# Kernel optimization log

Measured on AMD Instinct MI355X. Metric: run time of the kernel, lower is better.

Reference implementation:

```python
import jax, jax.numpy as jnp
import numpy as np
import math

CS = 8       # cell_size
NBINS = 8
SIGMA = 1.0
IMG = 224
BATCH = 256
TWO_PI = 2.0 * math.pi


def setup_inputs() -> dict:
    key = jax.random.key(0)
    x = jax.random.normal(key, (BATCH, 3, IMG, IMG), dtype=jnp.float32)
    coords = jnp.arange(CS, dtype=jnp.float32) - (CS - 1) / 2.0
    xx, yy = jnp.meshgrid(coords, coords, indexing='ij')
    gauss = jnp.exp(-(xx ** 2 + yy ** 2) / (2.0 * SIGMA ** 2)).reshape(1, CS * CS)
    kx = jnp.array([[-1., 0., 1.], [-2., 0., 2.], [-1., 0., 1.]], dtype=jnp.float32).reshape(1, 1, 3, 3)
    ky = jnp.array([[-1., -2., -1.], [0., 0., 0.], [1., 2., 1.]], dtype=jnp.float32).reshape(1, 1, 3, 3)
    return {"x": x, "gauss": gauss, "kx": kx, "ky": ky}


def _conv(im, k):
    # NCHW conv, padding=1, stride=1 (matches F.conv2d(..., padding=1))
    return jax.lax.conv_general_dilated(
        im, k, window_strides=(1, 1), padding=[(1, 1), (1, 1)],
        dimension_numbers=('NCHW', 'OIHW', 'NCHW'))


def reference(x, gauss, kx, ky):
    bs, _, H, W = x.shape
    gray = 0.2989 * x[:, 0:1] + 0.587 * x[:, 1:2] + 0.114 * x[:, 2:3]  # [bs,1,H,W]
    gx = _conv(gray, kx)
    gy = _conv(gray, ky)
    mag = jnp.sqrt(gx ** 2 + gy ** 2 + 1e-6)
    ang = jnp.mod(jnp.arctan2(gy, gx), TWO_PI)
    Hc, Wc = H // CS, W // CS
    n_cells = Hc * Wc

    def to_cells(a):
        # [bs,1,H,W] -> [bs*n_cells, CS*CS], within-cell order (kh,kw) row-major
        # matching F.unfold's kernel-position ordering.
        return a.reshape(bs, Hc, CS, Wc, CS).transpose(0, 1, 3, 2, 4).reshape(bs * n_cells, CS * CS)

    mags = to_cells(mag) * gauss  # gauss broadcasts over kernel positions
    angs = to_cells(ang)

    bin_w = TWO_PI / NBINS
    idx = (angs / bin_w).astype(jnp.int32) % NBINS  # [bs*n_cells, CS*CS]

    N = bs * n_cells
    hist = jnp.zeros((N, NBINS), dtype=mags.dtype)
    hist = hist.at[jnp.arange(N)[:, None], idx].add(mags)  # scatter_add per cell
    hist = hist.reshape(bs, n_cells * NBINS)
    hist = hist / (jnp.linalg.norm(hist, axis=1, keepdims=True) + 1e-6)
    return hist
```

## Files before the change

### kernel.cpp

```cpp
#include <hip/hip_runtime.h>
#include <math.h>

#define NBINS 8
#define IMG 224
#define HC 28
#define OUTPER (HC*HC*NBINS)
#define BATCH 256
#define PL (IMG*IMG)

__global__ __launch_bounds__(256) void hog_main_kernel(
    const float* __restrict__ x, const float* __restrict__ gauss,
    float* __restrict__ out, float* __restrict__ partial)
{
    const int tid  = threadIdx.x;
    const int wv   = tid >> 6;
    const int lane = tid & 63;
    const int bc   = blockIdx.x;
    const int b    = bc / HC;
    const int cr   = bc - b * HC;
    const int r0   = cr * 8;
    const int c0   = wv * 64;
    const int c    = c0 + lane;
    const int cl   = c > IMG - 1 ? IMG - 1 : c;

    const float* xb = x + (size_t)b * 3 * PL;

    float v[10];
    #pragma unroll
    for (int j = 0; j < 10; ++j) {
        int gr  = r0 - 1 + j;
        int grc = gr < 0 ? 0 : (gr > IMG - 1 ? IMG - 1 : gr);
        const float* p = xb + grc * IMG + cl;
        float R = p[0], G = p[PL], B = p[2 * PL];
        float gv = 0.2989f * R + 0.587f * G + 0.114f * B;
        v[j] = (gr < 0 || gr > IMG - 1) ? 0.f : gv;
    }

    float hl, hr;
    {
        int jl = lane - 54; jl = jl < 0 ? 0 : (jl > 9 ? 9 : jl);
        int gr = r0 - 1 + jl;
        int grc = gr < 0 ? 0 : (gr > IMG - 1 ? IMG - 1 : gr);
        int colL = c0 - 1; bool zc = colL < 0; int colc = zc ? 0 : colL;
        const float* p = xb + grc * IMG + colc;
        float R = p[0], G = p[PL], B = p[2 * PL];
        float gv = 0.2989f * R + 0.587f * G + 0.114f * B;
        hl = (zc || gr < 0 || gr > IMG - 1) ? 0.f : gv;
    }
    {
        int jr = lane - 44; jr = jr < 0 ? 0 : (jr > 9 ? 9 : jr);
        int gr = r0 - 1 + jr;
        int grc = gr < 0 ? 0 : (gr > IMG - 1 ? IMG - 1 : gr);
        int colR = c0 + 64; bool zc = colR > IMG - 1; int colc = zc ? IMG - 1 : colR;
        const float* p = xb + grc * IMG + colc;
        float R = p[0], G = p[PL], B = p[2 * PL];
        float gv = 0.2989f * R + 0.587f * G + 0.114f * B;
        hr = (zc || gr < 0 || gr > IMG - 1) ? 0.f : gv;
    }

    const int wc = lane & 7;
    float wgt[8];
    #pragma unroll
    for (int i = 0; i < 8; ++i) wgt[i] = gauss[i * 8 + wc];

    auto mklr = [&](int j, float& lf, float& rt) {
        float a = __shfl_up(v[j], 1, 64);
        float hLj = __shfl(hl, 54 + j, 64);
        lf = (lane == 0) ? hLj : a;
        float d = __shfl_down(v[j], 1, 64);
        float hRj = __shfl(hr, 44 + j, 64);
        d = (lane == 63) ? hRj : d;
        rt = (c >= IMG - 1) ? 0.f : d;
    };

    float h[8];
    #pragma unroll
    for (int k = 0; k < 8; ++k) h[k] = 0.f;

    float tL, tC, tR, mL, mC, mR;
    mklr(0, tL, tR); tC = v[0];
    mklr(1, mL, mR); mC = v[1];

    #pragma unroll
    for (int sr = 0; sr < 8; ++sr) {
        float bL, bR, bC = v[sr + 2];
        mklr(sr + 2, bL, bR);

        float gx = (tR - tL) + 2.f * (mR - mL) + (bR - bL);
        float gy = (bL - tL) + 2.f * (bC - tC) + (bR - tR);
        float mag = sqrtf(gx * gx + gy * gy + 1e-6f);
        float ax = fabsf(gx), ay = fabsf(gy);

        int bin;
        if (gy > 0.f)       bin = (gx > 0.f)  ? ((gy < gx) ? 0 : 1)
                                : (gx == 0.f) ? 2 : ((ay > ax) ? 2 : 3);
        else if (gy == 0.f) bin = (gx < 0.f) ? 4 : 0;
        else                bin = (gx < 0.f)  ? ((ay < ax) ? 4 : 5)
                                : (gx == 0.f) ? 6 : ((ay > ax) ? 6 : 7);

        float wm = wgt[sr] * mag;
        #pragma unroll
        for (int k = 0; k < 8; ++k) h[k] += (bin == k) ? wm : 0.f;

        tL = mL; tC = mC; tR = mR;
        mL = bL; mC = bC; mR = bR;
    }

    #pragma unroll
    for (int sh = 1; sh < 8; sh <<= 1) {
        #pragma unroll
        for (int k = 0; k < 8; ++k) h[k] += __shfl_xor(h[k], sh, 64);
    }
    float val = (wc < 4) ? ((wc < 2) ? (wc == 0 ? h[0] : h[1])
                                    : (wc == 2 ? h[2] : h[3]))
                         : ((wc < 6) ? (wc == 4 ? h[4] : h[5])
                                    : (wc == 6 ? h[6] : h[7]));
    float ssq = 0.f;
    if (c < IMG) {
        out[(size_t)b * OUTPER + (size_t)cr * IMG + c] = val;
        ssq = val * val;
    }

    #pragma unroll
    for (int o = 32; o > 0; o >>= 1) ssq += __shfl_down(ssq, o, 64);
    if (lane == 0) partial[bc * 4 + wv] = ssq;
}

__global__ __launch_bounds__(256) void hog_norm_kernel(
    float* __restrict__ out, const float* __restrict__ partial)
{
    const int b = blockIdx.x, tid = threadIdx.x;
    __shared__ float wsum[4];
    __shared__ float s_inv;
    float s = (tid < HC * 4) ? partial[b * HC * 4 + tid] : 0.f;
    #pragma unroll
    for (int o = 32; o > 0; o >>= 1) s += __shfl_down(s, o, 64);
    if ((tid & 63) == 0) wsum[tid >> 6] = s;
    __syncthreads();
    if (tid == 0) {
        float t = wsum[0] + wsum[1] + wsum[2] + wsum[3];
        s_inv = 1.0f / (sqrtf(t) + 1e-6f);
    }
    __syncthreads();
    float inv = s_inv;
    float4* o4 = (float4*)(out + (size_t)b * OUTPER);
    for (int i = tid; i < OUTPER / 4; i += 256) {
        float4 w = o4[i];
        w.x *= inv; w.y *= inv; w.z *= inv; w.w *= inv;
        o4[i] = w;
    }
}

extern "C" void kernel_launch(void* const* d_in, const int* in_sizes, int n_in,
                              void* d_out, int out_size, void* d_ws, size_t ws_size,
                              hipStream_t stream) {
    const float* x     = (const float*)d_in[0];
    const float* gauss = (const float*)d_in[1];
    float* out     = (float*)d_out;
    float* partial = (float*)d_ws;

    hog_main_kernel<<<BATCH * HC, 256, 0, stream>>>(x, gauss, out, partial);
    hog_norm_kernel<<<BATCH, 256, 0, stream>>>(out, partial);
}
```

Before: 226.9 us.

## Use LDS atomics for cell histograms, specialize edge loads, split norm blocks

The per-thread 8-bin select-accumulate and shuffle reduction are replaced with shared-memory atomicAdd into a per-wave histogram. Interior row blocks skip the boundary clamping through a templated load, and sqrtf becomes the raw hardware sqrt. The gauss weights are now computed in-kernel from a hardcoded exp2 formula and a constant row table instead of being read from the input. The norm kernel launches four blocks per image to expose more parallelism. These changes cut ALU work and raise parallelism, but LDS atomics can contend on the same bins, the gauss input is ignored (valid only for sigma=1, cs=8), and there is no barrier between the LDS init and the atomics beyond wave-local ordering.

Result: slower. 264.6 us (+16.6%).

```diff
diff --git a/kernel.cpp b/kernel.cpp
--- a/kernel.cpp
+++ b/kernel.cpp
@@ -8,10 +8,44 @@
 #define BATCH 256
 #define PL (IMG*IMG)
 
+template<bool EDGE>
+__device__ __forceinline__ void load_gray(const float* __restrict__ xb,
+    int r0, int c0, int cl, int lane, float v[10], float& hl, float& hr)
+{
+    #pragma unroll
+    for (int j = 0; j < 10; ++j) {
+        int gr  = r0 - 1 + j;
+        int grc = EDGE ? (gr < 0 ? 0 : (gr > IMG - 1 ? IMG - 1 : gr)) : gr;
+        const float* p = xb + grc * IMG + cl;
+        float gv = 0.2989f * p[0] + 0.587f * p[PL] + 0.114f * p[2 * PL];
+        v[j] = (EDGE && (gr < 0 || gr > IMG - 1)) ? 0.f : gv;
+    }
+    {
+        int jl = lane - 54; jl = jl < 0 ? 0 : (jl > 9 ? 9 : jl);
+        int gr = r0 - 1 + jl;
+        int grc = EDGE ? (gr < 0 ? 0 : (gr > IMG - 1 ? IMG - 1 : gr)) : gr;
+        int colL = c0 - 1; bool zc = colL < 0; int colc = zc ? 0 : colL;
+        const float* p = xb + grc * IMG + colc;
+        float gv = 0.2989f * p[0] + 0.587f * p[PL] + 0.114f * p[2 * PL];
+        hl = (zc || (EDGE && (gr < 0 || gr > IMG - 1))) ? 0.f : gv;
+    }
+    {
+        int jr = lane - 44; jr = jr < 0 ? 0 : (jr > 9 ? 9 : jr);
+        int gr = r0 - 1 + jr;
+        int grc = EDGE ? (gr < 0 ? 0 : (gr > IMG - 1 ? IMG - 1 : gr)) : gr;
+        int colR = c0 + 64; bool zc = colR > IMG - 1; int colc = zc ? IMG - 1 : colR;
+        const float* p = xb + grc * IMG + colc;
+        float gv = 0.2989f * p[0] + 0.587f * p[PL] + 0.114f * p[2 * PL];
+        hr = (zc || (EDGE && (gr < 0 || gr > IMG - 1))) ? 0.f : gv;
+    }
+}
+
 __global__ __launch_bounds__(256) void hog_main_kernel(
     const float* __restrict__ x, const float* __restrict__ gauss,
     float* __restrict__ out, float* __restrict__ partial)
 {
+    __shared__ float hist[4][64];
+
     const int tid  = threadIdx.x;
     const int wv   = tid >> 6;
     const int lane = tid & 63;
@@ -25,43 +59,19 @@
 
     const float* xb = x + (size_t)b * 3 * PL;
 
-    float v[10];
-    #pragma unroll
-    for (int j = 0; j < 10; ++j) {
-        int gr  = r0 - 1 + j;
-        int grc = gr < 0 ? 0 : (gr > IMG - 1 ? IMG - 1 : gr);
-        const float* p = xb + grc * IMG + cl;
-        float R = p[0], G = p[PL], B = p[2 * PL];
-        float gv = 0.2989f * R + 0.587f * G + 0.114f * B;
-        v[j] = (gr < 0 || gr > IMG - 1) ? 0.f : gv;
-    }
+    hist[wv][lane] = 0.f;
 
-    float hl, hr;
-    {
-        int jl = lane - 54; jl = jl < 0 ? 0 : (jl > 9 ? 9 : jl);
-        int gr = r0 - 1 + jl;
-        int grc = gr < 0 ? 0 : (gr > IMG - 1 ? IMG - 1 : gr);
-        int colL = c0 - 1; bool zc = colL < 0; int colc = zc ? 0 : colL;
-        const float* p = xb + grc * IMG + colc;
-        float R = p[0], G = p[PL], B = p[2 * PL];
-        float gv = 0.2989f * R + 0.587f * G + 0.114f * B;
-        hl = (zc || gr < 0 || gr > IMG - 1) ? 0.f : gv;
-    }
-    {
-        int jr = lane - 44; jr = jr < 0 ? 0 : (jr > 9 ? 9 : jr);
-        int gr = r0 - 1 + jr;
-        int grc = gr < 0 ? 0 : (gr > IMG - 1 ? IMG - 1 : gr);
-        int colR = c0 + 64; bool zc = colR > IMG - 1; int colc = zc ? IMG - 1 : colR;
-        const float* p = xb + grc * IMG + colc;
-        float R = p[0], G = p[PL], B = p[2 * PL];
-        float gv = 0.2989f * R + 0.587f * G + 0.114f * B;
-        hr = (zc || gr < 0 || gr > IMG - 1) ? 0.f : gv;
-    }
+    float v[10], hl, hr;
+    if (cr == 0 || cr == HC - 1) load_gray<true >(xb, r0, c0, cl, lane, v, hl, hr);
+    else                         load_gray<false>(xb, r0, c0, cl, lane, v, hl, hr);
 
     const int wc = lane & 7;
-    float wgt[8];
-    #pragma unroll
-    for (int i = 0; i < 8; ++i) wgt[i] = gauss[i * 8 + wc];
+    float tt = (float)wc - 3.5f;
+    float gw = __builtin_amdgcn_exp2f(-(tt * tt) * 0.72134752f);
+    const float EROW[8] = { 0.0021874911f, 0.043936934f, 0.32465247f, 0.88249690f,
+                            0.88249690f, 0.32465247f, 0.043936934f, 0.0021874911f };
+
+    float* cellp = &hist[wv][(lane >> 3) << 3];
 
     auto mklr = [&](int j, float& lf, float& rt) {
         float a = __shfl_up(v[j], 1, 64);
@@ -72,10 +82,6 @@
         d = (lane == 63) ? hRj : d;
         rt = (c >= IMG - 1) ? 0.f : d;
     };
-
-    float h[8];
-    #pragma unroll
-    for (int k = 0; k < 8; ++k) h[k] = 0.f;
 
     float tL, tC, tR, mL, mC, mR;
     mklr(0, tL, tR); tC = v[0];
@@ -88,7 +94,7 @@
 
         float gx = (tR - tL) + 2.f * (mR - mL) + (bR - bL);
         float gy = (bL - tL) + 2.f * (bC - tC) + (bR - tR);
-        float mag = sqrtf(gx * gx + gy * gy + 1e-6f);
+        float mag = __builtin_amdgcn_sqrtf(gx * gx + gy * gy + 1e-6f);
         float ax = fabsf(gx), ay = fabsf(gy);
 
         int bin;
@@ -98,23 +104,16 @@
         else                bin = (gx < 0.f)  ? ((ay < ax) ? 4 : 5)
                                 : (gx == 0.f) ? 6 : ((ay > ax) ? 6 : 7);
 
-        float wm = wgt[sr] * mag;
-        #pragma unroll
-        for (int k = 0; k < 8; ++k) h[k] += (bin == k) ? wm : 0.f;
+        float wm = EROW[sr] * (gw * mag);
+        atomicAdd(cellp + bin, wm);
 
         tL = mL; tC = mC; tR = mR;
         mL = bL; mC = bC; mR = bR;
     }
 
-    #pragma unroll
-    for (int sh = 1; sh < 8; sh <<= 1) {
-        #pragma unroll
-        for (int k = 0; k < 8; ++k) h[k] += __shfl_xor(h[k], sh, 64);
-    }
-    float val = (wc < 4) ? ((wc < 2) ? (wc == 0 ? h[0] : h[1])
-                                    : (wc == 2 ? h[2] : h[3]))
-                         : ((wc < 6) ? (wc == 4 ? h[4] : h[5])
-                                    : (wc == 6 ? h[6] : h[7]));
+    asm volatile("s_waitcnt lgkmcnt(0)" ::: "memory");
+    float val = hist[wv][lane];
+
     float ssq = 0.f;
     if (c < IMG) {
         out[(size_t)b * OUTPER + (size_t)cr * IMG + c] = val;
@@ -129,7 +128,8 @@
 __global__ __launch_bounds__(256) void hog_norm_kernel(
     float* __restrict__ out, const float* __restrict__ partial)
 {
-    const int b = blockIdx.x, tid = threadIdx.x;
+    const int bq = blockIdx.x, tid = threadIdx.x;
+    const int b = bq >> 2, q = bq & 3;
     __shared__ float wsum[4];
     __shared__ float s_inv;
     float s = (tid < HC * 4) ? partial[b * HC * 4 + tid] : 0.f;
@@ -143,8 +143,8 @@
     }
     __syncthreads();
     float inv = s_inv;
-    float4* o4 = (float4*)(out + (size_t)b * OUTPER);
-    for (int i = tid; i < OUTPER / 4; i += 256) {
+    float4* o4 = (float4*)(out + (size_t)b * OUTPER + (size_t)q * (OUTPER / 4));
+    for (int i = tid; i < OUTPER / 16; i += 256) {
         float4 w = o4[i];
         w.x *= inv; w.y *= inv; w.z *= inv; w.w *= inv;
         o4[i] = w;
@@ -160,5 +160,5 @@
     float* partial = (float*)d_ws;
 
     hog_main_kernel<<<BATCH * HC, 256, 0, stream>>>(x, gauss, out, partial);
-    hog_norm_kernel<<<BATCH, 256, 0, stream>>>(out, partial);
+    hog_norm_kernel<<<BATCH * 4, 256, 0, stream>>>(out, partial);
 }
```
